# Kernel tuning notes

Measured on AMD Instinct MI355X. Metric: run time of the kernel, lower is better.

The kernel has to match this reference:

```python
import jax, jax.numpy as jnp
import numpy as np

LENGTH = 500
DT = 0.1          # Euler step size
V0 = 0.02         # resting blood volume fraction (standard Balloon model)


def setup_inputs() -> dict:
    key = jax.random.key(0)
    noise = jax.random.normal(key, (LENGTH,), dtype=jnp.float32)
    return {
        "sigma": jnp.float32(0.5),
        "mu": jnp.float32(0.4),
        "lamb": jnp.float32(0.2),
        "beta": jnp.float32(0.5),
        "psi": jnp.float32(0.6),
        "phi": jnp.float32(1.5),
        "chi": jnp.float32(0.6),
        "noise": noise,
    }


def _euler_bold(sigma, mu, lamb, beta, psi, phi, chi, noise):
    """500-step Euler integration of neural state + Balloon-Windkessel
    hemodynamics (alpha = 1.0), with additive Gaussian noise on the neural
    state. Returns the BOLD time series, shape [LENGTH]."""
    dt = jnp.float32(DT)
    sqdt = jnp.sqrt(dt)
    k1 = 7.0 * beta
    k2 = jnp.float32(2.0)
    k3 = 2.0 * beta - 0.2

    def step(carry, eps):
        z, s, f, v, q = carry
        # neural state (Hopf-style cubic ODE) with injected noise
        dz = sigma * z - mu * z ** 3 + lamb
        z_n = z + dt * dz + sqdt * eps
        # hemodynamics (Balloon-Windkessel, alpha = 1 -> v**(1/alpha) == v)
        fv = v
        ds = z - phi * s - psi * (f - 1.0)
        df = s
        dv = (f - fv) / chi
        E = 1.0 - (1.0 - beta) ** (1.0 / f)   # oxygen extraction
        dq = (f * E / beta - fv * q / v) / chi
        s_n = s + dt * ds
        f_n = f + dt * df
        v_n = v + dt * dv
        q_n = q + dt * dq
        y = V0 * (k1 * (1.0 - q_n) + k2 * (1.0 - q_n / v_n) + k3 * (1.0 - v_n))
        return (z_n, s_n, f_n, v_n, q_n), y

    init = (jnp.float32(0.0), jnp.float32(0.0), jnp.float32(1.0),
            jnp.float32(1.0), jnp.float32(1.0))
    _, ys = jax.lax.scan(step, init, noise)
    return ys


def reference(sigma, mu, lamb, beta, psi, phi, chi, noise):
    yhat = _euler_bold(sigma, mu, lamb, beta, psi, phi, chi, noise)
    # torch.std defaults to unbiased (ddof=1)
    return yhat / jnp.std(yhat, ddof=1)
```

## Files before the change

### kernel.cpp

```cpp
#include <hip/hip_runtime.h>
#include <math.h>

#define LENGTH 500
#define NTHREADS 512

#if __has_builtin(__builtin_amdgcn_rcpf)
#define RCPF(x) __builtin_amdgcn_rcpf(x)
#else
#define RCPF(x) (1.0f / (x))
#endif
#if __has_builtin(__builtin_amdgcn_exp2f)
#define EXP2F(x) __builtin_amdgcn_exp2f(x)
#else
#define EXP2F(x) exp2f(x)
#endif

__global__ __launch_bounds__(NTHREADS) void bold_scan_kernel(
    const float* __restrict__ sigma_p, const float* __restrict__ mu_p,
    const float* __restrict__ lamb_p,  const float* __restrict__ beta_p,
    const float* __restrict__ psi_p,   const float* __restrict__ phi_p,
    const float* __restrict__ chi_p,   const float* __restrict__ noise,
    float* __restrict__ out)
{
    __shared__ float  dadd[512];
    __shared__ float4 qs4[125];
    __shared__ float4 vs4[125];
    __shared__ float  red[NTHREADS / 64];
    __shared__ float  bc[2];

    const int tid  = threadIdx.x;
    const int lane = tid & 63;
    const int wid  = tid >> 6;

    {
        const float dt   = 0.1f;
        const float sqdt = sqrtf(dt);
        const float dtl  = dt * lamb_p[0];
        float d = 0.0f;
        if (tid < LENGTH) d = fmaf(sqdt, noise[tid], dtl);
        dadd[tid] = d;
    }
    __syncthreads();

    if (tid == 0) {
        const float sigma = sigma_p[0];
        const float mu    = mu_p[0];
        const float beta  = beta_p[0];
        const float psi   = psi_p[0];
        const float phi   = phi_p[0];
        const float chi   = chi_p[0];

        const float dt     = 0.1f;
        const float ichi   = 1.0f / chi;
        const float dtichi = dt * ichi;
        const float cv     = 1.0f - dtichi;
        const float cs     = 1.0f - dt * phi;
        const float b2     = dt * psi;
        const float Aq     = dtichi / beta;
        const float l2b    = log2f(1.0f - beta);
        const float dtsig  = dt * sigma;
        const float ndtmu  = -dt * mu;

        float z = 0.0f, s = 0.0f, f = 1.0f, v = 1.0f, q = 1.0f;

#define STEP(D, QREF, VREF)                                                   \
        {                                                                     \
            float zD = z + (D);                                               \
            float z2 = z * z;                                                 \
            float z3 = z2 * z;                                                \
            float e  = fmaf(dtsig, z, zD);              \
            float zn = fmaf(ndtmu, z3, e);                                    \
            float inv_f = RCPF(f);                                            \
            float T  = EXP2F(l2b * inv_f);                                    \
            float fE = fmaf(-T, f, f);                             \
            float t1 = fmaf(-b2, f, b2);                    \
            float t2 = fmaf(dt, z, t1);                                       \
            float sn = fmaf(cs, s, t2);                                       \
            float fn = fmaf(dt, s, f);                                        \
            float vn = fmaf(dtichi, f, cv * v);                               \
            float qn = fmaf(cv, q, Aq * fE);                 \
            z = zn; s = sn; f = fn; v = vn; q = qn;                           \
            (QREF) = q; (VREF) = v;                                           \
        }

        const float4* dv4 = (const float4*)dadd;
        float4 curA = dv4[0];
        float4 curB = dv4[1];
        for (int i = 0; i < 496; i += 8) {
            float4 nextA = dv4[(i >> 2) + 2];
            float4 nextB = dv4[(i >> 2) + 3];
            float4 qA, vA, qB, vB;
            STEP(curA.x, qA.x, vA.x) STEP(curA.y, qA.y, vA.y)
            STEP(curA.z, qA.z, vA.z) STEP(curA.w, qA.w, vA.w)
            qs4[(i >> 2)]     = qA;  vs4[(i >> 2)]     = vA;
            STEP(curB.x, qB.x, vB.x) STEP(curB.y, qB.y, vB.y)
            STEP(curB.z, qB.z, vB.z) STEP(curB.w, qB.w, vB.w)
            qs4[(i >> 2) + 1] = qB;  vs4[(i >> 2) + 1] = vB;
            curA = nextA; curB = nextB;
        }
        {
            float4 qA, vA;
            STEP(curA.x, qA.x, vA.x) STEP(curA.y, qA.y, vA.y)
            STEP(curA.z, qA.z, vA.z) STEP(curA.w, qA.w, vA.w)
            qs4[124] = qA;  vs4[124] = vA;
        }
#undef STEP
    }
    __syncthreads();

    float y = 0.0f;
    {
        const float beta = beta_p[0];
        const float k1   = 7.0f * beta;
        const float k2   = 2.0f;
        const float k3   = 2.0f * beta - 0.2f;
        const float V0   = 0.02f;
        if (tid < LENGTH) {
            float q = ((const float*)qs4)[tid];
            float v = ((const float*)vs4)[tid];
            y = V0 * (k1 * (1.0f - q)
                    + k2 * (1.0f - q * RCPF(v))
                    + k3 * (1.0f - v));
        }
    }

    float sum = y;
    #pragma unroll
    for (int off = 32; off; off >>= 1) sum += __shfl_down(sum, off);
    if (lane == 0) red[wid] = sum;
    __syncthreads();
    if (tid == 0) {
        float t = 0.0f;
        #pragma unroll
        for (int w = 0; w < NTHREADS / 64; ++w) t += red[w];
        bc[0] = t / (float)LENGTH;
    }
    __syncthreads();

    const float mean = bc[0];
    float d = (tid < LENGTH) ? (y - mean) : 0.0f;
    float sq = d * d;
    #pragma unroll
    for (int off = 32; off; off >>= 1) sq += __shfl_down(sq, off);
    __syncthreads();
    if (lane == 0) red[wid] = sq;
    __syncthreads();
    if (tid == 0) {
        float t = 0.0f;
        #pragma unroll
        for (int w = 0; w < NTHREADS / 64; ++w) t += red[w];
        float var = t / (float)(LENGTH - 1);
        bc[1] = 1.0f / sqrtf(var);
    }
    __syncthreads();

    if (tid < LENGTH) out[tid] = y * bc[1];
}

extern "C" void kernel_launch(void* const* d_in, const int* in_sizes, int n_in,
                              void* d_out, int out_size, void* d_ws, size_t ws_size,
                              hipStream_t stream) {
    (void)in_sizes; (void)n_in; (void)d_ws; (void)ws_size; (void)out_size;
    const float* sigma = (const float*)d_in[0];
    const float* mu    = (const float*)d_in[1];
    const float* lamb  = (const float*)d_in[2];
    const float* beta  = (const float*)d_in[3];
    const float* psi   = (const float*)d_in[4];
    const float* phi   = (const float*)d_in[5];
    const float* chi   = (const float*)d_in[6];
    const float* noise = (const float*)d_in[7];
    float* out = (float*)d_out;

    bold_scan_kernel<<<1, NTHREADS, 0, stream>>>(
        sigma, mu, lamb, beta, psi, phi, chi, noise, out);
}
```

Before: 90.67 us.

## Decouple v/q recurrences into parallel affine scan over threads

The serial single-thread loop now integrates only z, s and f, storing f per step. Because v and q are linear recurrences driven by f, they are computed in parallel as an affine prefix scan: wave shuffles inside each wavefront, then a cross-wave combine through shared memory. This takes the exp2/rcp and the v/q updates off the serial critical path, shortening the dependent chain per step. In exchange it adds a scan phase, extra barriers, and a possible change in floating-point rounding order.

Measured after the change: 78.81 us. 13.1% less time.

```diff
diff --git a/kernel.cpp b/kernel.cpp
--- a/kernel.cpp
+++ b/kernel.cpp
@@ -22,11 +22,12 @@
     const float* __restrict__ chi_p,   const float* __restrict__ noise,
     float* __restrict__ out)
 {
-    __shared__ float  dadd[512];
-    __shared__ float4 qs4[125];
-    __shared__ float4 vs4[125];
-    __shared__ float  red[NTHREADS / 64];
-    __shared__ float  bc[2];
+    __shared__ float dadd[512];
+    __shared__ float fs[504];
+    __shared__ float wA[8], wBv[8], wBq[8];
+    __shared__ float pA[8], pBv[8], pBq[8];
+    __shared__ float red[8];
+    __shared__ float bc[2];
 
     const int tid  = threadIdx.x;
     const int lane = tid & 63;
@@ -45,83 +46,114 @@
     if (tid == 0) {
         const float sigma = sigma_p[0];
         const float mu    = mu_p[0];
-        const float beta  = beta_p[0];
         const float psi   = psi_p[0];
         const float phi   = phi_p[0];
-        const float chi   = chi_p[0];
-
-        const float dt     = 0.1f;
-        const float ichi   = 1.0f / chi;
-        const float dtichi = dt * ichi;
-        const float cv     = 1.0f - dtichi;
-        const float cs     = 1.0f - dt * phi;
-        const float b2     = dt * psi;
-        const float Aq     = dtichi / beta;
-        const float l2b    = log2f(1.0f - beta);
-        const float dtsig  = dt * sigma;
-        const float ndtmu  = -dt * mu;
-
-        float z = 0.0f, s = 0.0f, f = 1.0f, v = 1.0f, q = 1.0f;
-
-#define STEP(D, QREF, VREF)                                                   \
+
+        const float dt        = 0.1f;
+        const float cs        = 1.0f - dt * phi;
+        const float b2        = dt * psi;
+        const float nb2       = -b2;
+        const float onePdtsig = 1.0f + dt * sigma;
+        const float ndtmu     = -dt * mu;
+
+        float z = 0.0f, s = 0.0f, f = 1.0f;
+
+#define STEP(D, FREF)                                                         \
         {                                                                     \
-            float zD = z + (D);                                               \
             float z2 = z * z;                                                 \
-            float z3 = z2 * z;                                                \
-            float e  = fmaf(dtsig, z, zD);              \
-            float zn = fmaf(ndtmu, z3, e);                                    \
-            float inv_f = RCPF(f);                                            \
-            float T  = EXP2F(l2b * inv_f);                                    \
-            float fE = fmaf(-T, f, f);                             \
-            float t1 = fmaf(-b2, f, b2);                    \
+            float c  = fmaf(ndtmu, z2, onePdtsig);    \
+            float zn = fmaf(z, c, (D));                                       \
+            float t1 = fmaf(nb2, f, b2);                    \
             float t2 = fmaf(dt, z, t1);                                       \
             float sn = fmaf(cs, s, t2);                                       \
             float fn = fmaf(dt, s, f);                                        \
-            float vn = fmaf(dtichi, f, cv * v);                               \
-            float qn = fmaf(cv, q, Aq * fE);                 \
-            z = zn; s = sn; f = fn; v = vn; q = qn;                           \
-            (QREF) = q; (VREF) = v;                                           \
+            z = zn; s = sn; f = fn;                                           \
+            (FREF) = f;                                                       \
         }
 
         const float4* dv4 = (const float4*)dadd;
+        float4* fs4 = (float4*)fs;
         float4 curA = dv4[0];
         float4 curB = dv4[1];
         for (int i = 0; i < 496; i += 8) {
             float4 nextA = dv4[(i >> 2) + 2];
             float4 nextB = dv4[(i >> 2) + 3];
-            float4 qA, vA, qB, vB;
-            STEP(curA.x, qA.x, vA.x) STEP(curA.y, qA.y, vA.y)
-            STEP(curA.z, qA.z, vA.z) STEP(curA.w, qA.w, vA.w)
-            qs4[(i >> 2)]     = qA;  vs4[(i >> 2)]     = vA;
-            STEP(curB.x, qB.x, vB.x) STEP(curB.y, qB.y, vB.y)
-            STEP(curB.z, qB.z, vB.z) STEP(curB.w, qB.w, vB.w)
-            qs4[(i >> 2) + 1] = qB;  vs4[(i >> 2) + 1] = vB;
+            float4 fA, fB;
+            STEP(curA.x, fA.x) STEP(curA.y, fA.y)
+            STEP(curA.z, fA.z) STEP(curA.w, fA.w)
+            fs4[(i >> 2)] = fA;
+            STEP(curB.x, fB.x) STEP(curB.y, fB.y)
+            STEP(curB.z, fB.z) STEP(curB.w, fB.w)
+            fs4[(i >> 2) + 1] = fB;
             curA = nextA; curB = nextB;
         }
         {
-            float4 qA, vA;
-            STEP(curA.x, qA.x, vA.x) STEP(curA.y, qA.y, vA.y)
-            STEP(curA.z, qA.z, vA.z) STEP(curA.w, qA.w, vA.w)
-            qs4[124] = qA;  vs4[124] = vA;
+            float4 fA;
+            STEP(curA.x, fA.x) STEP(curA.y, fA.y)
+            STEP(curA.z, fA.z) STEP(curA.w, fA.w)
+            fs4[124] = fA;
         }
 #undef STEP
     }
     __syncthreads();
 
+    const float beta   = beta_p[0];
+    const float chi    = chi_p[0];
+    const float dt     = 0.1f;
+    const float dtichi = dt / chi;
+    const float cv     = 1.0f - dtichi;
+    const float Aq     = dtichi / beta;
+    const float l2b    = log2f(1.0f - beta);
+    const float k1     = 7.0f * beta;
+    const float k2     = 2.0f;
+    const float k3     = 2.0f * beta - 0.2f;
+    const float V0     = 0.02f;
+
+    float a = 1.0f, bv = 0.0f, bq = 0.0f;
+    if (tid < LENGTH) {
+        float fold = (tid == 0) ? 1.0f : fs[tid - 1];
+        float invf = RCPF(fold);
+        float T    = EXP2F(l2b * invf);
+        float fE   = fmaf(-T, fold, fold);
+        a  = cv;
+        bv = dtichi * fold;
+        bq = Aq * fE;
+    }
+    #pragma unroll
+    for (int off = 1; off < 64; off <<= 1) {
+        float ap  = __shfl_up(a,  off);
+        float bvp = __shfl_up(bv, off);
+        float bqp = __shfl_up(bq, off);
+        if (lane >= off) {
+            bv = fmaf(a, bvp, bv);
+            bq = fmaf(a, bqp, bq);
+            a  = a * ap;
+        }
+    }
+    if (lane == 63) { wA[wid] = a; wBv[wid] = bv; wBq[wid] = bq; }
+    __syncthreads();
+    if (tid == 0) {
+        float A = 1.0f, Bv = 0.0f, Bq = 0.0f;
+        #pragma unroll
+        for (int w = 0; w < 8; ++w) {
+            pA[w] = A; pBv[w] = Bv; pBq[w] = Bq;
+            Bv = fmaf(wA[w], Bv, wBv[w]);
+            Bq = fmaf(wA[w], Bq, wBq[w]);
+            A  = wA[w] * A;
+        }
+    }
+    __syncthreads();
+    float At  = a * pA[wid];
+    float Bvt = fmaf(a, pBv[wid], bv);
+    float Bqt = fmaf(a, pBq[wid], bq);
+    float v = At + Bvt;
+    float q = At + Bqt;
+
     float y = 0.0f;
-    {
-        const float beta = beta_p[0];
-        const float k1   = 7.0f * beta;
-        const float k2   = 2.0f;
-        const float k3   = 2.0f * beta - 0.2f;
-        const float V0   = 0.02f;
-        if (tid < LENGTH) {
-            float q = ((const float*)qs4)[tid];
-            float v = ((const float*)vs4)[tid];
-            y = V0 * (k1 * (1.0f - q)
-                    + k2 * (1.0f - q * RCPF(v))
-                    + k3 * (1.0f - v));
-        }
+    if (tid < LENGTH) {
+        y = V0 * (k1 * (1.0f - q)
+                + k2 * (1.0f - q * RCPF(v))
+                + k3 * (1.0f - v));
     }
 
     float sum = y;
@@ -132,7 +164,7 @@
     if (tid == 0) {
         float t = 0.0f;
         #pragma unroll
-        for (int w = 0; w < NTHREADS / 64; ++w) t += red[w];
+        for (int w = 0; w < 8; ++w) t += red[w];
         bc[0] = t / (float)LENGTH;
     }
     __syncthreads();
@@ -148,7 +180,7 @@
     if (tid == 0) {
         float t = 0.0f;
         #pragma unroll
-        for (int w = 0; w < NTHREADS / 64; ++w) t += red[w];
+        for (int w = 0; w < 8; ++w) t += red[w];
         float var = t / (float)(LENGTH - 1);
         bc[1] = 1.0f / sqrtf(var);
     }
```
